# Performance work log

Measured on AMD Instinct MI355X. Metric: run time of the kernel, lower is better.

The kernel has to match this reference:

```python
import jax, jax.numpy as jnp
import numpy as np

B = 2048
NU, NF, NA = 20000, 100000, 20000  # users, feeds, authors
D = 150   # SVD embed dim for FM features
DK = 64   # tag/keyword/d2v embed dim


def setup_inputs() -> dict:
    key = jax.random.key(0)
    ks = jax.random.split(key, 24)
    r = lambda k, shape: (jax.random.normal(k, shape, dtype=jnp.float32) * 0.05)
    # ids: user, feed, author columns with their own vocab ranges
    u = jax.random.randint(ks[0], (B,), 0, NU)
    f = jax.random.randint(ks[1], (B,), 0, NF)
    a = jax.random.randint(ks[2], (B,), 0, NA)
    inputs = jnp.stack([u, f, a], axis=1).astype(jnp.int32)  # [B,3]
    first_order_shifts = jnp.array([0, NU, NU + NF], dtype=jnp.int32)
    return {
        'inputs': inputs,
        'first_order_shifts': first_order_shifts,
        'W_user_feed': r(ks[3], (NU, D)),
        'W_feed_user': r(ks[4], (NF, D)),
        'W_user_author': r(ks[5], (NU, D)),
        'W_author_user': r(ks[6], (NA, D)),
        'W_feed_emb': r(ks[7], (NF, D)),          # trainable=False in original
        'W_user_tag': r(ks[8], (NU, DK)),
        'W_user_key1': r(ks[9], (NU, DK)),
        'W_user_key2': r(ks[10], (NU, DK)),
        'W_feed_tag': r(ks[11], (NF, DK)),
        'W_feed_key1': r(ks[12], (NF, DK)),
        'W_feed_key2': r(ks[13], (NF, DK)),
        'W_uf_d2v': r(ks[14], (NU, DK)),
        'W_fu_d2v': r(ks[15], (NF, DK)),
        'W_ua_d2v': r(ks[16], (NU, DK)),
        'W_au_d2v': r(ks[17], (NA, DK)),
        'W256': r(ks[18], (2 * D * D, 256)),       # 45000 -> 256
        'b256': jnp.zeros((256,), jnp.float32),
        'W128': r(ks[19], (2 * DK * DK, 128)),     # 8192 -> 128
        'b128': jnp.zeros((128,), jnp.float32),
    }


def reference(inputs, first_order_shifts, W_user_feed, W_feed_user,
              W_user_author, W_author_user, W_feed_emb, W_user_tag,
              W_user_key1, W_user_key2, W_feed_tag, W_feed_key1, W_feed_key2,
              W_uf_d2v, W_fu_d2v, W_ua_d2v, W_au_d2v, W256, b256, W128, b128):
    inputs = inputs.reshape(-1, 3)
    u, f, a = inputs[:, 0], inputs[:, 1], inputs[:, 2]
    one_hot_inputs = inputs + first_order_shifts[None, :]

    user_feed_embed = W_user_feed[u]      # [B,150]
    user_author_embed = W_user_author[u]
    author_user_embed = W_author_user[a]
    feed_emb_embed = W_feed_emb[f]
    feed_user_embed = W_feed_user[f]
    user_tag_embed = W_user_tag[u]        # [B,64]
    user_key1_embed = W_user_key1[u]
    user_key2_embed = W_user_key2[u]
    feed_tag_embed = W_feed_tag[f]
    feed_key1_embed = W_feed_key1[f]
    feed_key2_embed = W_feed_key2[f]
    user_feed_d2vem = W_uf_d2v[u]
    user_author_d2vem = W_ua_d2v[u]
    feed_user_d2vem = W_fu_d2v[f]
    author_user_d2vem = W_au_d2v[a]

    # d2v outer products -> [B,64,64] each; concat axis=1 -> [B,128,64]
    user_w_feed = jnp.einsum('bi,bj->bij', user_feed_d2vem, feed_user_d2vem)
    user_w_auth = jnp.einsum('bi,bj->bij', user_author_d2vem, author_user_d2vem)
    user_w_user = jnp.concatenate([user_w_feed, user_w_auth], axis=1)
    user_w_user = user_w_user.reshape(-1, 2 * DK * DK)
    user_w_user = jax.nn.relu(user_w_user @ W128 + b128)  # Dropout inactive (inference)

    # SVD outer products -> [B,150,150] each; concat axis=1 -> [B,300,150]
    user_x_feed = jnp.einsum('bi,bj->bij', user_feed_embed, feed_user_embed)
    user_x_auth = jnp.einsum('bi,bj->bij', user_author_embed, author_user_embed)
    user_x_user = jnp.concatenate([user_x_feed, user_x_auth], axis=1)
    user_x_user = user_x_user.reshape(-1, 2 * D * D)
    user_x_user = jax.nn.relu(user_x_user @ W256 + b256)

    # tf.concat([list], axis=1) stacks the inner list -> [4,B,150], then reshape (-1,4,150)
    embeds_fm = jnp.stack([user_feed_embed, user_author_embed,
                           feed_user_embed, author_user_embed], axis=0)
    fm_embed_inputs = embeds_fm.reshape(-1, 4, D)

    expert_inputs = jnp.concatenate([
        user_feed_embed, user_author_embed, user_tag_embed, user_key1_embed,
        user_key2_embed, user_feed_d2vem, user_author_d2vem, feed_user_embed,
        feed_tag_embed, feed_key1_embed, feed_emb_embed, feed_key2_embed,
        feed_user_d2vem, author_user_embed, author_user_d2vem,
        user_x_user, user_w_user], axis=-1)  # [B,1710]
    return expert_inputs, one_hot_inputs, fm_embed_inputs
```

## Files before the change

### kernel.cpp

```cpp
#include <hip/hip_runtime.h>
#include <hip/hip_bf16.h>
#include <stdint.h>

#define BB   2048
#define DD   150
#define DKK  64

static constexpr int EXPERT_W  = 1774;
static constexpr int X_OFF     = 1390;
static constexpr int W_OFF     = 1646;
static constexpr int EXPERT_SZ = BB * EXPERT_W;
static constexpr int OH_BASE   = EXPERT_SZ;
static constexpr int FM_BASE   = OH_BASE + BB * 3;

static constexpr size_t WTX_OFF = 0;
static constexpr size_t WTW_OFF = 24576000;
static constexpr size_t WSX_OFF = 26673152;
static constexpr size_t WSW_OFF = 60227584;
static constexpr size_t WS_NEED = 77004800;

typedef __attribute__((ext_vector_type(8))) short bf16x8;
typedef __attribute__((ext_vector_type(4))) float f32x4;

union APack { int d[4]; bf16x8 v; };

__device__ __forceinline__ int cvtpk_bf16(float a, float b) {
  int r; asm("v_cvt_pk_bf16_f32 %0, %1, %2" : "=v"(r) : "v"(a), "v"(b)); return r;
}
__device__ __forceinline__ f32x4 mfma16(bf16x8 a, bf16x8 b, f32x4 c) {
  return __builtin_amdgcn_mfma_f32_16x16x32_bf16(a, b, c, 0, 0, 0);
}
__device__ __forceinline__ void gload16(const void* g, void* l) {
  __builtin_amdgcn_global_load_lds(
      (__attribute__((address_space(1))) void*)(g),
      (__attribute__((address_space(3))) void*)(l), 16, 0, 0);
}

__global__ __launch_bounds__(256) void gather_kernel(
    const int* __restrict__ inputs, const int* __restrict__ shifts,
    const float* __restrict__ Wuf, const float* __restrict__ Wfu,
    const float* __restrict__ Wua, const float* __restrict__ Wau,
    const float* __restrict__ Wfe,
    const float* __restrict__ Wut, const float* __restrict__ Wuk1, const float* __restrict__ Wuk2,
    const float* __restrict__ Wft, const float* __restrict__ Wfk1, const float* __restrict__ Wfk2,
    const float* __restrict__ Wufd, const float* __restrict__ Wfud,
    const float* __restrict__ Wuad, const float* __restrict__ Waud,
    float* __restrict__ out)
{
    const int b = blockIdx.x;
    const int u = inputs[b*3 + 0];
    const int f = inputs[b*3 + 1];
    const int a = inputs[b*3 + 2];
    float* row = out + b * EXPERT_W;
    float* fm  = out + FM_BASE;
    const int t = threadIdx.x;

    for (int c = t; c < DD; c += 256) {
        float ufe = Wuf[u*DD + c];
        float uae = Wua[u*DD + c];
        float fue = Wfu[f*DD + c];
        float fee = Wfe[f*DD + c];
        float aue = Wau[a*DD + c];
        row[0    + c] = ufe;
        row[150  + c] = uae;
        row[620  + c] = fue;
        row[898  + c] = fee;
        row[1176 + c] = aue;
        fm[0*BB*DD + b*DD + c] = ufe;
        fm[1*BB*DD + b*DD + c] = uae;
        fm[2*BB*DD + b*DD + c] = fue;
        fm[3*BB*DD + b*DD + c] = aue;
    }
    for (int c = t; c < DKK; c += 256) {
        row[300  + c] = Wut [u*DKK + c];
        row[364  + c] = Wuk1[u*DKK + c];
        row[428  + c] = Wuk2[u*DKK + c];
        row[492  + c] = Wufd[u*DKK + c];
        row[556  + c] = Wuad[u*DKK + c];
        row[770  + c] = Wft [f*DKK + c];
        row[834  + c] = Wfk1[f*DKK + c];
        row[1048 + c] = Wfk2[f*DKK + c];
        row[1112 + c] = Wfud[f*DKK + c];
        row[1326 + c] = Waud[a*DKK + c];
    }
    if (t < 3) {
        out[OH_BASE + b*3 + t] = (float)(inputs[b*3 + t] + shifts[t]);
    }
}

__global__ __launch_bounds__(256) void tile_pack_x(
    const float* __restrict__ W, __hip_bfloat16* __restrict__ Wt)
{
  const int T  = blockIdx.x;
  const int jj = T / 300;
  const int i  = T - jj*300;
  const int t  = threadIdx.x;
  float v[32];
  const float* src = W + ((size_t)i*150 + jj*32)*256 + t;
  #pragma unroll
  for (int jl = 0; jl < 32; ++jl) {
    int j = jj*32 + jl;
    v[jl] = (j < 150) ? src[(size_t)jl*256] : 0.f;
  }
  const int blk = t >> 4, nloc = t & 15;
  char* dst = (char*)Wt + (size_t)T*16384 + (size_t)(blk*512 + nloc*8)*2;
  #pragma unroll
  for (int ksub = 0; ksub < 4; ++ksub) {
    int pk0 = cvtpk_bf16(v[ksub*8+0], v[ksub*8+1]);
    int pk1 = cvtpk_bf16(v[ksub*8+2], v[ksub*8+3]);
    int pk2 = cvtpk_bf16(v[ksub*8+4], v[ksub*8+5]);
    int pk3 = cvtpk_bf16(v[ksub*8+6], v[ksub*8+7]);
    *(int4*)(dst + (size_t)ksub*256) = make_int4(pk0, pk1, pk2, pk3);
  }
}

__global__ __launch_bounds__(128) void tile_pack_w(
    const float* __restrict__ W, __hip_bfloat16* __restrict__ Wt)
{
  const int T  = blockIdx.x;
  const int jj = T >> 7;
  const int i  = T & 127;
  const int t  = threadIdx.x;
  float v[32];
  const float* src = W + ((size_t)i*64 + jj*32)*128 + t;
  #pragma unroll
  for (int jl = 0; jl < 32; ++jl) v[jl] = src[(size_t)jl*128];
  const int blk = t >> 4, nloc = t & 15;
  char* dst = (char*)Wt + (size_t)T*8192 + (size_t)(blk*512 + nloc*8)*2;
  #pragma unroll
  for (int ksub = 0; ksub < 4; ++ksub) {
    int pk0 = cvtpk_bf16(v[ksub*8+0], v[ksub*8+1]);
    int pk1 = cvtpk_bf16(v[ksub*8+2], v[ksub*8+3]);
    int pk2 = cvtpk_bf16(v[ksub*8+4], v[ksub*8+5]);
    int pk3 = cvtpk_bf16(v[ksub*8+6], v[ksub*8+7]);
    *(int4*)(dst + (size_t)ksub*256) = make_int4(pk0, pk1, pk2, pk3);
  }
}

__global__ __launch_bounds__(512, 4) void xuser_mfma(
    const int* __restrict__ inputs,
    const float* __restrict__ Wuf, const float* __restrict__ Wua,
    const float* __restrict__ Wfu, const float* __restrict__ Wau,
    const __hip_bfloat16* __restrict__ WtXt, float* __restrict__ wsX)
{
  __shared__ float xlds[128*20];
  __shared__ __align__(16) __hip_bfloat16 blds[2][8192];

  const int bid = blockIdx.x;
  const int h  = bid & 1;
  const int s  = (bid >> 1) & 15;
  const int mb = bid >> 5;
  const int b0 = mb * 128;
  const bool upper = s >= 8;
  const int sl  = upper ? s - 8 : s;
  const int i0l = sl * 19;
  const int cnt = (150 - i0l) < 19 ? (150 - i0l) : 19;
  const int ig0 = i0l + (upper ? 150 : 0);
  const int tid = threadIdx.x;

  const float* X = upper ? Wua : Wuf;
  const float* Y = upper ? Wau : Wfu;
  const int yoff = upper ? 2 : 1;

  for (int k = tid; k < 128*20; k += 512) {
    int r = k / 20, ii = k - r*20;
    float v = 0.f;
    if (ii < cnt) v = X[(size_t)inputs[(b0+r)*3]*150 + i0l + ii];
    xlds[k] = v;
  }

  const int lane = tid & 63;
  const int w  = tid >> 6;
  const int mg = w >> 1;
  const int ng = w & 1;
  const int lr = lane & 15;
  const int g  = lane >> 4;

  int yid[2];
  #pragma unroll
  for (int mf = 0; mf < 2; ++mf)
    yid[mf] = inputs[(size_t)(b0 + mg*32 + mf*16 + lr)*3 + yoff];

  const char* wtb = (const char*)WtXt + (size_t)h*8192;
  const unsigned wdst = (unsigned)(tid & ~63) * 16;

  f32x4 acc[2][4];
  #pragma unroll
  for (int i = 0; i < 2; ++i)
    #pragma unroll
    for (int j = 0; j < 4; ++j) acc[i][j] = (f32x4){0.f,0.f,0.f,0.f};

  auto stage = [&](int bufi, int T, int c2) {
    const char* sp = wtb + (size_t)T*16384 + (size_t)tid*16;
    char* dp = (char*)&blds[bufi][0] + wdst;
    gload16(sp, dp);
    if (c2 > 1) gload16(sp + 16384, dp + 8192);
  };

  auto computeSub = [&](const __hip_bfloat16* bb, int ii) {
    bf16x8 bv[4];
    #pragma unroll
    for (int nf = 0; nf < 4; ++nf)
      bv[nf] = *(const bf16x8*)(bb + (ng*4 + nf)*512 + g*128 + lr*8);
    APack a[2];
    #pragma unroll
    for (int mf = 0; mf < 2; ++mf) {
      float xv = xlds[(mg*32 + mf*16 + lr)*20 + ii];
      float* yr = nullptr; (void)yr;
      #pragma unroll
      for (int e = 0; e < 4; ++e)
        a[mf].d[e] = cvtpk_bf16(xv*0.f, xv*0.f);
    }
    return bv[0];
  };
  (void)computeSub;

  stage(0, ig0, cnt >= 2 ? 2 : 1);
  __syncthreads();

  int buf = 0;
  for (int jj = 0; jj < 5; ++jj) {
    float yreg[2][8];
    const int jb = jj*32 + g*8;
    #pragma unroll
    for (int mf = 0; mf < 2; ++mf) {
      const float* yp = Y + (size_t)yid[mf]*150;
      if (jb + 8 <= 150) {
        #pragma unroll
        for (int hh = 0; hh < 4; ++hh) {
          float2 vv = *(const float2*)(yp + jb + 2*hh);
          yreg[mf][2*hh]   = vv.x;
          yreg[mf][2*hh+1] = vv.y;
        }
      } else {
        #pragma unroll
        for (int e = 0; e < 8; ++e)
          yreg[mf][e] = (jb + e < 150) ? yp[jb + e] : 0.f;
      }
    }
    for (int ii = 0; ii < cnt; ii += 2) {
      const int rem = cnt - ii;
      int njj = jj, nii = ii + 2;
      if (nii >= cnt) { njj++; nii = 0; }
      if (njj < 5) stage(buf^1, njj*300 + ig0 + nii, (cnt - nii) >= 2 ? 2 : 1);

      #pragma unroll
      for (int sc = 0; sc < 2; ++sc) {
        if (sc == 1 && rem < 2) break;
        const __hip_bfloat16* bb = &blds[buf][sc*4096];
        bf16x8 bv[4];
        #pragma unroll
        for (int nf = 0; nf < 4; ++nf)
          bv[nf] = *(const bf16x8*)(bb + (ng*4 + nf)*512 + g*128 + lr*8);
        APack a[2];
        #pragma unroll
        for (int mf = 0; mf < 2; ++mf) {
          float xv = xlds[(mg*32 + mf*16 + lr)*20 + ii + sc];
          #pragma unroll
          for (int e = 0; e < 4; ++e)
            a[mf].d[e] = cvtpk_bf16(xv*yreg[mf][2*e], xv*yreg[mf][2*e+1]);
        }
        #pragma unroll
        for (int mf = 0; mf < 2; ++mf)
          #pragma unroll
          for (int nf = 0; nf < 4; ++nf)
            acc[mf][nf] = mfma16(a[mf].v, bv[nf], acc[mf][nf]);
      }
      __syncthreads();
      buf ^= 1;
    }
  }

  float* wp = wsX + ((size_t)s*2048 + b0)*256;
  #pragma unroll
  for (int mf = 0; mf < 2; ++mf) {
    #pragma unroll
    for (int nf = 0; nf < 4; ++nf) {
      int rb  = mg*32 + mf*16 + g*4;
      int col = h*128 + ng*64 + nf*16 + lr;
      f32x4 v = acc[mf][nf];
      #pragma unroll
      for (int e = 0; e < 4; ++e) wp[(size_t)(rb+e)*256 + col] = v[e];
    }
  }
}

__global__ __launch_bounds__(512, 4) void wuser_mfma(
    const int* __restrict__ inputs,
    const float* __restrict__ Wufd, const float* __restrict__ Wuad,
    const float* __restrict__ Wfud, const float* __restrict__ Waud,
    const __hip_bfloat16* __restrict__ WtWt, float* __restrict__ wsW)
{
  __shared__ float xlds[128*8];
  __shared__ __align__(16) __hip_bfloat16 blds[2][8192];

  const int mb = blockIdx.x >> 4;
  const int s  = blockIdx.x & 15;
  const int b0 = mb * 128;
  const bool upper = s >= 8;
  const int i0l = (s & 7) * 8;
  const int ig0 = i0l + (upper ? 64 : 0);
  const int tid = threadIdx.x;

  const float* X = upper ? Wuad : Wufd;
  const float* Y = upper ? Waud : Wfud;
  const int yoff = upper ? 2 : 1;

  for (int k = tid; k < 128*8; k += 512) {
    int r = k >> 3, ii = k & 7;
    xlds[k] = X[(size_t)inputs[(size_t)(b0+r)*3]*64 + i0l + ii];
  }

  const int lane = tid & 63;
  const int w  = tid >> 6;
  const int mg = w >> 1;
  const int ng = w & 1;
  const int lr = lane & 15;
  const int g  = lane >> 4;

  int yid[2];
  #pragma unroll
  for (int mf = 0; mf < 2; ++mf)
    yid[mf] = inputs[(size_t)(b0 + mg*32 + mf*16 + lr)*3 + yoff];

  const char* wtb = (const char*)WtWt;
  const unsigned wdst = (unsigned)(tid & ~63) * 16;

  f32x4 acc[2][4];
  #pragma unroll
  for (int i = 0; i < 2; ++i)
    #pragma unroll
    for (int j = 0; j < 4; ++j) acc[i][j] = (f32x4){0.f,0.f,0.f,0.f};

  auto stage = [&](int bufi, int T) {
    const char* sp = wtb + (size_t)T*8192 + (size_t)tid*16;
    char* dp = (char*)&blds[bufi][0] + wdst;
    gload16(sp, dp);
    gload16(sp + 8192, dp + 8192);
  };

  stage(0, ig0);
  __syncthreads();

  int buf = 0;
  for (int jj = 0; jj < 2; ++jj) {
    float yreg[2][8];
    const int jb = jj*32 + g*8;
    #pragma unroll
    for (int mf = 0; mf < 2; ++mf) {
      const float* yp = Y + (size_t)yid[mf]*64 + jb;
      #pragma unroll
      for (int hh = 0; hh < 2; ++hh) {
        float4 v = *(const float4*)(yp + hh*4);
        yreg[mf][hh*4]   = v.x;
        yreg[mf][hh*4+1] = v.y;
        yreg[mf][hh*4+2] = v.z;
        yreg[mf][hh*4+3] = v.w;
      }
    }
    for (int ii = 0; ii < 8; ii += 2) {
      int njj = jj, nii = ii + 2;
      if (nii >= 8) { njj++; nii = 0; }
      if (njj < 2) stage(buf^1, njj*128 + ig0 + nii);

      #pragma unroll
      for (int sc = 0; sc < 2; ++sc) {
        const __hip_bfloat16* bb = &blds[buf][sc*4096];
        bf16x8 bv[4];
        #pragma unroll
        for (int nf = 0; nf < 4; ++nf)
          bv[nf] = *(const bf16x8*)(bb + (ng*4 + nf)*512 + g*128 + lr*8);
        APack a[2];
        #pragma unroll
        for (int mf = 0; mf < 2; ++mf) {
          float xv = xlds[(mg*32 + mf*16 + lr)*8 + ii + sc];
          #pragma unroll
          for (int e = 0; e < 4; ++e)
            a[mf].d[e] = cvtpk_bf16(xv*yreg[mf][2*e], xv*yreg[mf][2*e+1]);
        }
        #pragma unroll
        for (int mf = 0; mf < 2; ++mf)
          #pragma unroll
          for (int nf = 0; nf < 4; ++nf)
            acc[mf][nf] = mfma16(a[mf].v, bv[nf], acc[mf][nf]);
      }
      __syncthreads();
      buf ^= 1;
    }
  }

  float* wp = wsW + ((size_t)s*2048 + b0)*128;
  #pragma unroll
  for (int mf = 0; mf < 2; ++mf) {
    #pragma unroll
    for (int nf = 0; nf < 4; ++nf) {
      int rb  = mg*32 + mf*16 + g*4;
      int col = ng*64 + nf*16 + lr;
      f32x4 v = acc[mf][nf];
      #pragma unroll
      for (int e = 0; e < 4; ++e) wp[(size_t)(rb+e)*128 + col] = v[e];
    }
  }
}

__global__ __launch_bounds__(256) void epilogue_kernel(
    const float* __restrict__ wsX, const float* __restrict__ wsW,
    const float* __restrict__ b256, const float* __restrict__ b128,
    float* __restrict__ out)
{
  int idx = blockIdx.x*256 + threadIdx.x;
  if (idx >= BB*384) return;
  int b = idx / 384, c = idx - b*384;
  if (c < 256) {
    float acc = b256[c];
    #pragma unroll
    for (int k = 0; k < 16; ++k) acc += wsX[((size_t)k*BB + b)*256 + c];
    out[(size_t)b*EXPERT_W + X_OFF + c] = acc > 0.f ? acc : 0.f;
  } else {
    int cc = c - 256;
    float acc = b128[cc];
    #pragma unroll
    for (int k = 0; k < 16; ++k) acc += wsW[((size_t)k*BB + b)*128 + cc];
    out[(size_t)b*EXPERT_W + W_OFF + cc] = acc > 0.f ? acc : 0.f;
  }
}

static constexpr int NPAIR_X = 300 * 150;
static constexpr int CHX     = 128;

__global__ __launch_bounds__(256) void xuser_kernel(
    const int* __restrict__ inputs,
    const float* __restrict__ Wuf, const float* __restrict__ Wua,
    const float* __restrict__ Wfu, const float* __restrict__ Wau,
    const float* __restrict__ W256, const float* __restrict__ b256,
    float* __restrict__ out)
{
    __shared__ float xs[16][308];
    __shared__ float ys[16][308];
    __shared__ float xy[CHX][16];
    const int half = blockIdx.x & 1;
    const int bg   = blockIdx.x >> 1;
    const int b0   = bg * 16;
    const int t    = threadIdx.x;
    const int bl   = t & 15;
    const int kg   = t >> 4;
    const int kbase = half * 128 + kg * 8;
    for (int idx = t; idx < 16 * DD; idx += 256) {
        int bb = idx / DD;
        int c  = idx - bb * DD;
        int u = inputs[(b0+bb)*3 + 0];
        int f = inputs[(b0+bb)*3 + 1];
        int a = inputs[(b0+bb)*3 + 2];
        xs[bb][c]       = Wuf[u*DD + c];
        xs[bb][150 + c] = Wua[u*DD + c];
        ys[bb][c]       = Wfu[f*DD + c];
        ys[bb][150 + c] = Wau[a*DD + c];
    }
    float acc[8] = {0,0,0,0,0,0,0,0};
    for (int base = 0; base < NPAIR_X; base += CHX) {
        __syncthreads();
        #pragma unroll
        for (int r = 0; r < (CHX*16)/256; ++r) {
            int idx = t + r * 256;
            int pl  = idx >> 4;
            int bb  = idx & 15;
            int p   = base + pl;
            if (p < NPAIR_X) {
                int i = p / 150;
                int j = p - i * 150;
                xy[pl][bb] = xs[bb][i] * ys[bb][(i >= 150 ? 150 : 0) + j];
            }
        }
        __syncthreads();
        const int lim = min(CHX, NPAIR_X - base);
        const float* wp = W256 + base * 256 + kbase;
        for (int pl = 0; pl < lim; ++pl) {
            float sv = xy[pl][bl];
            const float4* w4 = (const float4*)(wp + pl * 256);
            float4 w0 = w4[0], w1 = w4[1];
            acc[0] = fmaf(sv, w0.x, acc[0]); acc[1] = fmaf(sv, w0.y, acc[1]);
            acc[2] = fmaf(sv, w0.z, acc[2]); acc[3] = fmaf(sv, w0.w, acc[3]);
            acc[4] = fmaf(sv, w1.x, acc[4]); acc[5] = fmaf(sv, w1.y, acc[5]);
            acc[6] = fmaf(sv, w1.z, acc[6]); acc[7] = fmaf(sv, w1.w, acc[7]);
        }
    }
    const int rowbase = (b0 + bl) * EXPERT_W + X_OFF;
    #pragma unroll
    for (int m = 0; m < 8; ++m) {
        float v = acc[m] + b256[kbase + m];
        out[rowbase + kbase + m] = (v > 0.f ? v : 0.f);
    }
}

static constexpr int NPAIR_W = 128 * 64;
static constexpr int CHW     = 256;

__global__ __launch_bounds__(256) void wuser_kernel(
    const int* __restrict__ inputs,
    const float* __restrict__ Wufd, const float* __restrict__ Wuad,
    const float* __restrict__ Wfud, const float* __restrict__ Waud,
    const float* __restrict__ W128, const float* __restrict__ b128,
    float* __restrict__ out)
{
    __shared__ float xs[8][132];
    __shared__ float ys[8][132];
    __shared__ float xy[CHW][8];
    const int bg = blockIdx.x;
    const int b0 = bg * 8;
    const int t  = threadIdx.x;
    const int bl = t & 7;
    const int kg = t >> 3;
    const int kbase = kg * 4;
    for (int idx = t; idx < 8 * DKK; idx += 256) {
        int bb = idx >> 6;
        int c  = idx & 63;
        int u = inputs[(b0+bb)*3 + 0];
        int f = inputs[(b0+bb)*3 + 1];
        int a = inputs[(b0+bb)*3 + 2];
        xs[bb][c]      = Wufd[u*DKK + c];
        xs[bb][64 + c] = Wuad[u*DKK + c];
        ys[bb][c]      = Wfud[f*DKK + c];
        ys[bb][64 + c] = Waud[a*DKK + c];
    }
    float acc[4] = {0,0,0,0};
    for (int base = 0; base < NPAIR_W; base += CHW) {
        __syncthreads();
        #pragma unroll
        for (int r = 0; r < (CHW*8)/256; ++r) {
            int idx = t + r * 256;
            int pl  = idx >> 3;
            int bb  = idx & 7;
            int p   = base + pl;
            int i = p >> 6;
            int j = p & 63;
            xy[pl][bb] = xs[bb][i] * ys[bb][(i >= 64 ? 64 : 0) + j];
        }
        __syncthreads();
        const float* wp = W128 + base * 128 + kbase;
        for (int pl = 0; pl < CHW; ++pl) {
            float sv = xy[pl][bl];
            float4 wv = *(const float4*)(wp + pl * 128);
            acc[0] = fmaf(sv, wv.x, acc[0]); acc[1] = fmaf(sv, wv.y, acc[1]);
            acc[2] = fmaf(sv, wv.z, acc[2]); acc[3] = fmaf(sv, wv.w, acc[3]);
        }
    }
    const int rowbase = (b0 + bl) * EXPERT_W + W_OFF;
    #pragma unroll
    for (int m = 0; m < 4; ++m) {
        float v = acc[m] + b128[kbase + m];
        out[rowbase + kbase + m] = (v > 0.f ? v : 0.f);
    }
}

extern "C" void kernel_launch(void* const* d_in, const int* in_sizes, int n_in,
                              void* d_out, int out_size, void* d_ws, size_t ws_size,
                              hipStream_t stream)
{
    const int*   inputs = (const int*)  d_in[0];
    const int*   shifts = (const int*)  d_in[1];
    const float* Wuf    = (const float*)d_in[2];
    const float* Wfu    = (const float*)d_in[3];
    const float* Wua    = (const float*)d_in[4];
    const float* Wau    = (const float*)d_in[5];
    const float* Wfe    = (const float*)d_in[6];
    const float* Wut    = (const float*)d_in[7];
    const float* Wuk1   = (const float*)d_in[8];
    const float* Wuk2   = (const float*)d_in[9];
    const float* Wft    = (const float*)d_in[10];
    const float* Wfk1   = (const float*)d_in[11];
    const float* Wfk2   = (const float*)d_in[12];
    const float* Wufd   = (const float*)d_in[13];
    const float* Wfud   = (const float*)d_in[14];
    const float* Wuad   = (const float*)d_in[15];
    const float* Waud   = (const float*)d_in[16];
    const float* W256   = (const float*)d_in[17];
    const float* b256   = (const float*)d_in[18];
    const float* W128   = (const float*)d_in[19];
    const float* b128   = (const float*)d_in[20];

    float* out = (float*)d_out;

    gather_kernel<<<BB, 256, 0, stream>>>(inputs, shifts,
        Wuf, Wfu, Wua, Wau, Wfe, Wut, Wuk1, Wuk2, Wft, Wfk1, Wfk2,
        Wufd, Wfud, Wuad, Waud, out);

    if (ws_size >= WS_NEED) {
        char* ws = (char*)d_ws;
        __hip_bfloat16* WtX = (__hip_bfloat16*)(ws + WTX_OFF);
        __hip_bfloat16* WtW = (__hip_bfloat16*)(ws + WTW_OFF);
        float* wsX = (float*)(ws + WSX_OFF);
        float* wsW = (float*)(ws + WSW_OFF);

        tile_pack_x<<<1500, 256, 0, stream>>>(W256, WtX);
        tile_pack_w<<<256, 128, 0, stream>>>(W128, WtW);

        xuser_mfma<<<512, 512, 0, stream>>>(inputs, Wuf, Wua, Wfu, Wau, WtX, wsX);
        wuser_mfma<<<256, 512, 0, stream>>>(inputs, Wufd, Wuad, Wfud, Waud, WtW, wsW);

        epilogue_kernel<<<(BB*384 + 255)/256, 256, 0, stream>>>(wsX, wsW, b256, b128, out);
    } else {
        xuser_kernel<<<256, 256, 0, stream>>>(inputs, Wuf, Wua, Wfu, Wau, W256, b256, out);
        wuser_kernel<<<256, 256, 0, stream>>>(inputs, Wufd, Wuad, Wfud, Waud, W128, b128, out);
    }
}
```

Before: 105.8 us.

## Deepen weight-tile prefetch to two stages with explicit vmcnt waits

Rewrites the K-loop of both outer-product MFMA kernels into a single flattened loop that keeps two LDS weight tiles in flight. Each tile is issued two iterations ahead. Full __syncthreads is replaced by s_waitcnt vmcnt plus raw s_barrier and a sched_barrier. The goal is to hide global-to-LDS load latency behind MFMA work instead of exposing it on every iteration. In exchange, the hand-counted vmcnt is fragile when the Y-row loads interleave with the tile loads, and the second chunk is now always loaded even for odd counts.

```diff
diff --git a/kernel.cpp b/kernel.cpp
--- a/kernel.cpp
+++ b/kernel.cpp
@@ -184,91 +184,86 @@
   const char* wtb = (const char*)WtXt + (size_t)h*8192;
   const unsigned wdst = (unsigned)(tid & ~63) * 16;
 
-  f32x4 acc[2][4];
-  #pragma unroll
-  for (int i = 0; i < 2; ++i)
-    #pragma unroll
-    for (int j = 0; j < 4; ++j) acc[i][j] = (f32x4){0.f,0.f,0.f,0.f};
-
-  auto stage = [&](int bufi, int T, int c2) {
+  auto stageT = [&](int bufi, int T) {
     const char* sp = wtb + (size_t)T*16384 + (size_t)tid*16;
     char* dp = (char*)&blds[bufi][0] + wdst;
-    gload16(sp, dp);
-    if (c2 > 1) gload16(sp + 16384, dp + 8192);
+    gload16(sp,         dp);
+    gload16(sp + 16384, dp + 8192);
   };
 
-  auto computeSub = [&](const __hip_bfloat16* bb, int ii) {
-    bf16x8 bv[4];
-    #pragma unroll
-    for (int nf = 0; nf < 4; ++nf)
-      bv[nf] = *(const bf16x8*)(bb + (ng*4 + nf)*512 + g*128 + lr*8);
-    APack a[2];
-    #pragma unroll
-    for (int mf = 0; mf < 2; ++mf) {
-      float xv = xlds[(mg*32 + mf*16 + lr)*20 + ii];
-      float* yr = nullptr; (void)yr;
-      #pragma unroll
-      for (int e = 0; e < 4; ++e)
-        a[mf].d[e] = cvtpk_bf16(xv*0.f, xv*0.f);
-    }
-    return bv[0];
-  };
-  (void)computeSub;
-
-  stage(0, ig0, cnt >= 2 ? 2 : 1);
-  __syncthreads();
-
-  int buf = 0;
-  for (int jj = 0; jj < 5; ++jj) {
-    float yreg[2][8];
-    const int jb = jj*32 + g*8;
-    #pragma unroll
-    for (int mf = 0; mf < 2; ++mf) {
-      const float* yp = Y + (size_t)yid[mf]*150;
-      if (jb + 8 <= 150) {
+  f32x4 acc[2][4];
+  #pragma unroll
+  for (int i = 0; i < 2; ++i)
+    #pragma unroll
+    for (int j = 0; j < 4; ++j) acc[i][j] = (f32x4){0.f,0.f,0.f,0.f};
+
+  const int PJ = (cnt + 1) >> 1;
+  const int P  = 5 * PJ;
+
+  stageT(0, ig0);
+  stageT(1, ig0 + 2);
+
+  int jjc = 0, iic = 0;
+  int jjs = 0, iis = 4;
+  int yjj = -1;
+  float yreg[2][8];
+
+  for (int p = 0; p < P; ++p) {
+    if (jjc != yjj) {
+      yjj = jjc;
+      const int jb = jjc*32 + g*8;
+      #pragma unroll
+      for (int mf = 0; mf < 2; ++mf) {
+        const float* yp = Y + (size_t)yid[mf]*150;
+        if (jb + 8 <= 150) {
+          #pragma unroll
+          for (int hh = 0; hh < 4; ++hh) {
+            float2 vv = *(const float2*)(yp + jb + 2*hh);
+            yreg[mf][2*hh]   = vv.x;
+            yreg[mf][2*hh+1] = vv.y;
+          }
+        } else {
+          #pragma unroll
+          for (int e = 0; e < 8; ++e)
+            yreg[mf][e] = (jb + e < 150) ? yp[jb + e] : 0.f;
+        }
+      }
+    }
+    if (p + 1 < P) asm volatile("s_waitcnt vmcnt(2)" ::: "memory");
+    else           asm volatile("s_waitcnt vmcnt(0)" ::: "memory");
+    __builtin_amdgcn_s_barrier();
+    __builtin_amdgcn_sched_barrier(0);
+
+    const int buf = p & 1;
+    const int rem = cnt - iic;
+    #pragma unroll
+    for (int sc = 0; sc < 2; ++sc) {
+      if (sc == 1 && rem < 2) break;
+      const __hip_bfloat16* bb = &blds[buf][sc*4096];
+      bf16x8 bv[4];
+      #pragma unroll
+      for (int nf = 0; nf < 4; ++nf)
+        bv[nf] = *(const bf16x8*)(bb + (ng*4 + nf)*512 + g*128 + lr*8);
+      APack a[2];
+      #pragma unroll
+      for (int mf = 0; mf < 2; ++mf) {
+        float xv = xlds[(mg*32 + mf*16 + lr)*20 + iic + sc];
         #pragma unroll
-        for (int hh = 0; hh < 4; ++hh) {
-          float2 vv = *(const float2*)(yp + jb + 2*hh);
-          yreg[mf][2*hh]   = vv.x;
-          yreg[mf][2*hh+1] = vv.y;
-        }
-      } else {
-        #pragma unroll
-        for (int e = 0; e < 8; ++e)
-          yreg[mf][e] = (jb + e < 150) ? yp[jb + e] : 0.f;
+        for (int e = 0; e < 4; ++e)
+          a[mf].d[e] = cvtpk_bf16(xv*yreg[mf][2*e], xv*yreg[mf][2*e+1]);
       }
-    }
-    for (int ii = 0; ii < cnt; ii += 2) {
-      const int rem = cnt - ii;
-      int njj = jj, nii = ii + 2;
-      if (nii >= cnt) { njj++; nii = 0; }
-      if (njj < 5) stage(buf^1, njj*300 + ig0 + nii, (cnt - nii) >= 2 ? 2 : 1);
-
-      #pragma unroll
-      for (int sc = 0; sc < 2; ++sc) {
-        if (sc == 1 && rem < 2) break;
-        const __hip_bfloat16* bb = &blds[buf][sc*4096];
-        bf16x8 bv[4];
+      #pragma unroll
+      for (int mf = 0; mf < 2; ++mf)
         #pragma unroll
         for (int nf = 0; nf < 4; ++nf)
-          bv[nf] = *(const bf16x8*)(bb + (ng*4 + nf)*512 + g*128 + lr*8);
-        APack a[2];
-        #pragma unroll
-        for (int mf = 0; mf < 2; ++mf) {
-          float xv = xlds[(mg*32 + mf*16 + lr)*20 + ii + sc];
-          #pragma unroll
-          for (int e = 0; e < 4; ++e)
-            a[mf].d[e] = cvtpk_bf16(xv*yreg[mf][2*e], xv*yreg[mf][2*e+1]);
-        }
-        #pragma unroll
-        for (int mf = 0; mf < 2; ++mf)
-          #pragma unroll
-          for (int nf = 0; nf < 4; ++nf)
-            acc[mf][nf] = mfma16(a[mf].v, bv[nf], acc[mf][nf]);
-      }
-      __syncthreads();
-      buf ^= 1;
-    }
+          acc[mf][nf] = mfma16(a[mf].v, bv[nf], acc[mf][nf]);
+    }
+
+    __builtin_amdgcn_s_barrier();
+    if (p + 2 < P) stageT(buf, jjs*300 + ig0 + iis);
+
+    iic += 2; if (iic >= cnt) { iic = 0; ++jjc; }
+    iis += 2; if (iis >= cnt) { iis = 0; ++jjs; }
   }
 
   float* wp = wsX + ((size_t)s*2048 + b0)*256;
@@ -326,67 +321,77 @@
   const char* wtb = (const char*)WtWt;
   const unsigned wdst = (unsigned)(tid & ~63) * 16;
 
-  f32x4 acc[2][4];
-  #pragma unroll
-  for (int i = 0; i < 2; ++i)
-    #pragma unroll
-    for (int j = 0; j < 4; ++j) acc[i][j] = (f32x4){0.f,0.f,0.f,0.f};
-
-  auto stage = [&](int bufi, int T) {
+  auto stageT = [&](int bufi, int T) {
     const char* sp = wtb + (size_t)T*8192 + (size_t)tid*16;
     char* dp = (char*)&blds[bufi][0] + wdst;
-    gload16(sp, dp);
+    gload16(sp,        dp);
     gload16(sp + 8192, dp + 8192);
   };
 
-  stage(0, ig0);
-  __syncthreads();
-
-  int buf = 0;
-  for (int jj = 0; jj < 2; ++jj) {
-    float yreg[2][8];
-    const int jb = jj*32 + g*8;
-    #pragma unroll
-    for (int mf = 0; mf < 2; ++mf) {
-      const float* yp = Y + (size_t)yid[mf]*64 + jb;
-      #pragma unroll
-      for (int hh = 0; hh < 2; ++hh) {
-        float4 v = *(const float4*)(yp + hh*4);
-        yreg[mf][hh*4]   = v.x;
-        yreg[mf][hh*4+1] = v.y;
-        yreg[mf][hh*4+2] = v.z;
-        yreg[mf][hh*4+3] = v.w;
+  f32x4 acc[2][4];
+  #pragma unroll
+  for (int i = 0; i < 2; ++i)
+    #pragma unroll
+    for (int j = 0; j < 4; ++j) acc[i][j] = (f32x4){0.f,0.f,0.f,0.f};
+
+  stageT(0, ig0);
+  stageT(1, ig0 + 2);
+
+  int jjc = 0, iic = 0;
+  int jjs = 0, iis = 4;
+  int yjj = -1;
+  float yreg[2][8];
+
+  for (int p = 0; p < 8; ++p) {
+    if (jjc != yjj) {
+      yjj = jjc;
+      const int jb = jjc*32 + g*8;
+      #pragma unroll
+      for (int mf = 0; mf < 2; ++mf) {
+        const float* yp = Y + (size_t)yid[mf]*64 + jb;
+        #pragma unroll
+        for (int hh = 0; hh < 2; ++hh) {
+          float4 v = *(const float4*)(yp + hh*4);
+          yreg[mf][hh*4]   = v.x;
+          yreg[mf][hh*4+1] = v.y;
+          yreg[mf][hh*4+2] = v.z;
+          yreg[mf][hh*4+3] = v.w;
+        }
       }
     }
-    for (int ii = 0; ii < 8; ii += 2) {
-      int njj = jj, nii = ii + 2;
-      if (nii >= 8) { njj++; nii = 0; }
-      if (njj < 2) stage(buf^1, njj*128 + ig0 + nii);
-
-      #pragma unroll
-      for (int sc = 0; sc < 2; ++sc) {
-        const __hip_bfloat16* bb = &blds[buf][sc*4096];
-        bf16x8 bv[4];
+    if (p + 1 < 8) asm volatile("s_waitcnt vmcnt(2)" ::: "memory");
+    else           asm volatile("s_waitcnt vmcnt(0)" ::: "memory");
+    __builtin_amdgcn_s_barrier();
+    __builtin_amdgcn_sched_barrier(0);
+
+    const int buf = p & 1;
+    #pragma unroll
+    for (int sc = 0; sc < 2; ++sc) {
+      const __hip_bfloat16* bb = &blds[buf][sc*4096];
+      bf16x8 bv[4];
+      #pragma unroll
+      for (int nf = 0; nf < 4; ++nf)
+        bv[nf] = *(const bf16x8*)(bb + (ng*4 + nf)*512 + g*128 + lr*8);
+      APack a[2];
+      #pragma unroll
+      for (int mf = 0; mf < 2; ++mf) {
+        float xv = xlds[(mg*32 + mf*16 + lr)*8 + iic + sc];
+        #pragma unroll
+        for (int e = 0; e < 4; ++e)
+          a[mf].d[e] = cvtpk_bf16(xv*yreg[mf][2*e], xv*yreg[mf][2*e+1]);
+      }
+      #pragma unroll
+      for (int mf = 0; mf < 2; ++mf)
         #pragma unroll
         for (int nf = 0; nf < 4; ++nf)
-          bv[nf] = *(const bf16x8*)(bb + (ng*4 + nf)*512 + g*128 + lr*8);
-        APack a[2];
-        #pragma unroll
-        for (int mf = 0; mf < 2; ++mf) {
-          float xv = xlds[(mg*32 + mf*16 + lr)*8 + ii + sc];
-          #pragma unroll
-          for (int e = 0; e < 4; ++e)
-            a[mf].d[e] = cvtpk_bf16(xv*yreg[mf][2*e], xv*yreg[mf][2*e+1]);
-        }
-        #pragma unroll
-        for (int mf = 0; mf < 2; ++mf)
-          #pragma unroll
-          for (int nf = 0; nf < 4; ++nf)
-            acc[mf][nf] = mfma16(a[mf].v, bv[nf], acc[mf][nf]);
-      }
-      __syncthreads();
-      buf ^= 1;
-    }
+          acc[mf][nf] = mfma16(a[mf].v, bv[nf], acc[mf][nf]);
+    }
+
+    __builtin_amdgcn_s_barrier();
+    if (p + 2 < 8) stageT(buf, jjs*128 + ig0 + iis);
+
+    iic += 2; if (iic >= 8) { iic = 0; ++jjc; }
+    iis += 2; if (iis >= 8) { iis = 0; ++jjs; }
   }
 
   float* wp = wsW + ((size_t)s*2048 + b0)*128;
```

New measurement: 105.7 us. Within noise of the previous version (-0.0%).
